# Kernel tuning notes

Hardware: AMD Instinct MI355X
Metric: run time of the kernel (lower is better)

Reference implementation:

```python
import jax, jax.numpy as jnp
import numpy as np

N, E, ND, ED, H, OUT, L, VC = 10000, 160000, 8, 4, 128, 256, 6, 6
HEADS, C = 4, 128  # GATConv: out_channels=128 per head, concat=False -> mean over heads


def _ln(x, g, b, eps=1e-5):
    m = x.mean(-1, keepdims=True)
    v = ((x - m) ** 2).mean(-1, keepdims=True)
    return (x - m) * jax.lax.rsqrt(v + eps) * g + b


def _gat_layer(h, src, dst, e_attr, lw, a_src, a_dst, lew, a_edge, bias):
    # h: [N,H]; e_attr: [Etot,H]; PyG GATConv(heads=4, concat=False, edge_dim=H)
    xh = (h @ lw).reshape(N, HEADS, C)                 # [N,4,128]
    eh = (e_attr @ lew).reshape(-1, HEADS, C)          # [Etot,4,128]
    al_s = jnp.einsum('nhc,hc->nh', xh, a_src)
    al_d = jnp.einsum('nhc,hc->nh', xh, a_dst)
    al_e = jnp.einsum('ehc,hc->eh', eh, a_edge)
    alpha = jax.nn.leaky_relu(al_s[src] + al_d[dst] + al_e, 0.2)  # [Etot,4]
    amax = jax.ops.segment_max(alpha, dst, num_segments=N)
    ex = jnp.exp(alpha - amax[dst])
    den = jax.ops.segment_sum(ex, dst, num_segments=N)
    w = ex / (den[dst] + 1e-16)
    out = jax.ops.segment_sum(xh[src] * w[..., None], dst, num_segments=N)  # [N,4,128]
    return out.mean(axis=1) + bias


def setup_inputs() -> dict:
    key = jax.random.key(0)
    ks = jax.random.split(key, 32)
    s = 0.05
    d = {
        'x': jax.random.normal(ks[0], (N, ND), jnp.float32),
        'edge_index': jax.random.randint(ks[1], (2, E), 0, N),
        'edge_attr': jax.random.uniform(ks[2], (E, ED), jnp.float32),
        'vnf_context': jax.random.normal(ks[3], (1, VC), jnp.float32),
        # node embedding
        'node_w': jax.random.normal(ks[4], (ND, H)) * s, 'node_b': jnp.zeros((H,)),
        # EdgeAttentionLayer
        'ea_proj_w': jax.random.normal(ks[5], (ED, H)) * s, 'ea_proj_b': jnp.zeros((H,)),
        'vnf_w': jax.random.normal(ks[6], (VC, H)) * s, 'vnf_b': jnp.zeros((H,)),
        'att1_w': jax.random.normal(ks[7], (2 * H, H)) * s, 'att1_b': jnp.zeros((H,)),
        'att2_w': jax.random.normal(ks[8], (H, H // 2)) * s, 'att2_b': jnp.zeros((H // 2,)),
        'att3_w': jax.random.normal(ks[9], (H // 2, 1)) * s, 'att3_b': jnp.zeros((1,)),
        # per-layer GATConv params (stacked over L layers)
        'gat_lin_w': jax.random.normal(ks[10], (L, H, HEADS * C)) * s,
        'gat_att_src': jax.random.normal(ks[11], (L, HEADS, C)) * s,
        'gat_att_dst': jax.random.normal(ks[12], (L, HEADS, C)) * s,
        'gat_lin_edge_w': jax.random.normal(ks[13], (L, H, HEADS * C)) * s,
        'gat_att_edge': jax.random.normal(ks[14], (L, HEADS, C)) * s,
        'gat_bias': jnp.zeros((L, C)),
        'ln_scale': jnp.ones((L, H)), 'ln_bias': jnp.zeros((L, H)),
        # output projection
        'out_w': jax.random.normal(ks[15], (H, OUT)) * s, 'out_b': jnp.zeros((OUT,)),
    }
    return d


def reference(x, edge_index, edge_attr, vnf_context, node_w, node_b, ea_proj_w, ea_proj_b,
              vnf_w, vnf_b, att1_w, att1_b, att2_w, att2_b, att3_w, att3_b,
              gat_lin_w, gat_att_src, gat_att_dst, gat_lin_edge_w, gat_att_edge, gat_bias,
              ln_scale, ln_bias, out_w, out_b):
    src, dst = edge_index[0], edge_index[1]
    h = x @ node_w + node_b                                   # [N,128]
    # EdgeAttentionLayer (eval mode, no network_state)
    ef = edge_attr @ ea_proj_w + ea_proj_b                    # [E,128]
    vnf = vnf_context @ vnf_w + vnf_b                         # [1,128]
    comb = jnp.concatenate([ef, jnp.broadcast_to(vnf, (E, H))], axis=-1)
    a = jax.nn.relu(comb @ att1_w + att1_b)
    a = jax.nn.relu(a @ att2_w + att2_b)
    e_gate = jax.nn.sigmoid(a @ att3_w + att3_b)              # [E,1]
    w_edge = ef * e_gate                                      # [E,128]
    # GATConv default add_self_loops=True, fill_value='mean'
    loop = jnp.arange(N)
    src2 = jnp.concatenate([src, loop])
    dst2 = jnp.concatenate([dst, loop])
    e2 = jnp.concatenate([w_edge, jnp.broadcast_to(w_edge.mean(0, keepdims=True), (N, H))], axis=0)
    for l in range(L):
        hc = _gat_layer(h, src2, dst2, e2, gat_lin_w[l], gat_att_src[l], gat_att_dst[l],
                        gat_lin_edge_w[l], gat_att_edge[l], gat_bias[l])
        h = _ln(h + jax.nn.relu(hc), ln_scale[l], ln_bias[l])
    return h @ out_w + out_b                                  # [N,256]
```

## Files before the change

### kernel.cpp

```cpp
#include <hip/hip_runtime.h>
#include <hip/hip_bf16.h>
#include <math.h>

#define Nn 10000
#define Ee 160000
#define ET 170000
#define LL 6

typedef short v8s __attribute__((ext_vector_type(8)));
typedef float v4f __attribute__((ext_vector_type(4)));

__device__ __forceinline__ unsigned short f2bf(float v) {
    unsigned int b = __float_as_uint(v);
    b += 0x7fffu + ((b >> 16) & 1u);
    return (unsigned short)(b >> 16);
}
__device__ __forceinline__ float bflo(unsigned int u) { return __uint_as_float(u << 16); }
__device__ __forceinline__ float bfhi(unsigned int u) { return __uint_as_float(u & 0xffff0000u); }

__global__ __launch_bounds__(256) void k_first(
    const float* __restrict__ x, const float* __restrict__ nw,
    const float* __restrict__ nb, float* __restrict__ h, unsigned short* __restrict__ hb,
    const int* __restrict__ ei, int* __restrict__ hist,
    const float* __restrict__ glw, const float* __restrict__ gas,
    const float* __restrict__ gad, const float* __restrict__ glew,
    const float* __restrict__ gae, float* __restrict__ Bs,
    float* __restrict__ Bd, float* __restrict__ Be,
    unsigned short* __restrict__ WsumT,
    const float* __restrict__ a2w, unsigned short* __restrict__ w2bf,
    const float* __restrict__ vnfc, const float* __restrict__ vw,
    const float* __restrict__ vb, const float* __restrict__ eab,
    const float* __restrict__ a1w, const float* __restrict__ a1b,
    const float* __restrict__ eaw, float* __restrict__ E1) {
    __shared__ float vr[128];
    __shared__ float sM1[512];
    __shared__ float sd1[128];
    int b = blockIdx.x, t = threadIdx.x;
    if (b < 5000) {
        int idx = b * 256 + t;
        int n = idx >> 7, c = idx & 127;
        const float* xr = x + (size_t)n * 8;
        float acc = nb[c];
#pragma unroll
        for (int k = 0; k < 8; k++) acc += xr[k] * nw[k * 128 + c];
        h[idx] = acc;
        hb[idx] = f2bf(acc);
        return;
    }
    if (b < 5665) {
        int i = (b - 5000) * 256 + t;
        if (i < ET) {
            int d = (i < Ee) ? ei[Ee + i] : (i - Ee);
            atomicAdd(&hist[d], 1);
        }
        return;
    }
    if (b < 5677) {
        int idx = (b - 5665) * 256 + t;
        if (idx >= LL * 128 * 4) return;
        int hh = idx & 3, k = (idx >> 2) & 127, l = idx >> 9;
        const float* lwp = glw  + (size_t)l * 65536 + k * 512 + hh * 128;
        const float* lep = glew + (size_t)l * 65536 + k * 512 + hh * 128;
        const float* sp = gas + l * 512 + hh * 128;
        const float* dp = gad + l * 512 + hh * 128;
        const float* ep = gae + l * 512 + hh * 128;
        float s1 = 0, s2 = 0, s3 = 0;
        for (int c = 0; c < 128; c++) {
            float lv = lwp[c];
            s1 += lv * sp[c];
            s2 += lv * dp[c];
            s3 += lep[c] * ep[c];
        }
        Bs[idx] = s1; Bd[idx] = s2; Be[idx] = s3;
        return;
    }
    if (b < 7213) {
        int idx = (b - 5677) * 256 + t;
        int kk = idx & 511;
        int c = (idx >> 9) & 127;
        int l = idx >> 16;
        float v = 0.25f * glw[(size_t)l * 65536 + (size_t)(kk & 127) * 512 + (kk >> 7) * 128 + c];
        WsumT[(size_t)l * 65536 + (size_t)c * 512 + kk] = f2bf(v);
        return;
    }
    if (b < 7245) {
        int idx = (b - 7213) * 256 + t;
        int j = idx & 7, lane = (idx >> 3) & 63, nt = (idx >> 9) & 3, ks = idx >> 11;
        int k = ks * 32 + ((lane >> 4) << 3) + j;
        int n = nt * 16 + (lane & 15);
        w2bf[idx] = f2bf(a2w[k * 64 + n]);
        return;
    }
    {
        if (t < 128) {
            float a = vb[t];
#pragma unroll
            for (int k = 0; k < 6; k++) a += vnfc[k] * vw[k * 128 + t];
            vr[t] = a;
        }
        __syncthreads();
        if (t < 128) {
            float a = a1b[t];
            for (int k = 0; k < 128; k++) a += eab[k] * a1w[k * 128 + t];
            for (int k = 0; k < 128; k++) a += vr[k] * a1w[(128 + k) * 128 + t];
            sd1[t] = a;
        }
#pragma unroll
        for (int rr = 0; rr < 2; rr++) {
            int id = rr * 256 + t;
            int r = id >> 7, j = id & 127;
            float a = 0.f;
            for (int k = 0; k < 128; k++) a += eaw[r * 128 + k] * a1w[k * 128 + j];
            sM1[id] = a;
        }
        __syncthreads();
        if (t < 128) {
            E1[t * 8 + 0] = sM1[t];
            E1[t * 8 + 1] = sM1[128 + t];
            E1[t * 8 + 2] = sM1[256 + t];
            E1[t * 8 + 3] = sM1[384 + t];
            E1[t * 8 + 4] = sd1[t];
            E1[t * 8 + 5] = 0.f; E1[t * 8 + 6] = 0.f; E1[t * 8 + 7] = 0.f;
        }
    }
}

__global__ __launch_bounds__(1024) void k_scan(
    const int* __restrict__ hist, int* __restrict__ seg, int* __restrict__ pos,
    const float* __restrict__ eaw, const float* __restrict__ eab,
    const float* __restrict__ Be, float* __restrict__ PB, float* __restrict__ cB) {
    __shared__ int wsums[16];
    __shared__ int carry_s;
    int t = threadIdx.x;
    if (blockIdx.x == 1) {
        if (t >= 24) return;
        int l = t >> 2, hh = t & 3;
        const float* bp = Be + l * 512 + hh;
        float s0 = 0, s1 = 0, s2 = 0, s3 = 0, sc = 0;
        for (int k = 0; k < 128; k++) {
            float bv = bp[k * 4];
            s0 += eaw[0 * 128 + k] * bv;
            s1 += eaw[1 * 128 + k] * bv;
            s2 += eaw[2 * 128 + k] * bv;
            s3 += eaw[3 * 128 + k] * bv;
            sc += eab[k] * bv;
        }
        PB[0 * 24 + t] = s0; PB[1 * 24 + t] = s1;
        PB[2 * 24 + t] = s2; PB[3 * 24 + t] = s3;
        cB[t] = sc;
        return;
    }
    int lane = t & 63, wid = t >> 6;
    if (t == 0) { carry_s = 0; seg[0] = 0; }
    __syncthreads();
    for (int base = 0; base < Nn; base += 1024) {
        int idx = base + t;
        int v = (idx < Nn) ? hist[idx] : 0;
        int sc = v;
#pragma unroll
        for (int d = 1; d < 64; d <<= 1) {
            int up = __shfl_up(sc, d);
            if (lane >= d) sc += up;
        }
        if (lane == 63) wsums[wid] = sc;
        __syncthreads();
        if (wid == 0) {
            int wv = (lane < 16) ? wsums[lane] : 0;
            int wsc = wv;
#pragma unroll
            for (int d = 1; d < 16; d <<= 1) {
                int up = __shfl_up(wsc, d);
                if (lane >= d) wsc += up;
            }
            if (lane < 16) wsums[lane] = wsc - wv;
        }
        __syncthreads();
        int carry = carry_s;
        int inc = sc + wsums[wid] + carry;
        if (idx < Nn) { seg[idx + 1] = inc; pos[idx] = inc - v; }
        __syncthreads();
        if (t == 1023) carry_s = inc;
        __syncthreads();
    }
}

__global__ __launch_bounds__(256, 2) void k_edge(
    const float* __restrict__ ea, const float* __restrict__ E1,
    const unsigned short* __restrict__ w2bf,
    const float* __restrict__ a2b, const float* __restrict__ a3w,
    const float* __restrict__ a3b,
    const float* __restrict__ PB, const float* __restrict__ cB,
    const int* __restrict__ ei, int* __restrict__ pos, int* __restrict__ srcv,
    float* __restrict__ aleT, float* __restrict__ gsum) {
    __shared__ float4 sM[128];
    __shared__ float sD[128];
    __shared__ float4 sevs[256];
    __shared__ float gsh[256];
    __shared__ float sgsum[5];
    int t = threadIdx.x;
    int lane = t & 63;
    int wid = t >> 6;
    int c = lane & 15, q = lane >> 4;
    int eb0 = blockIdx.x * 256;

    int my_src = ei[eb0 + t];
    int my_dst = ei[Ee + eb0 + t];
    sevs[t] = *(const float4*)(ea + (size_t)(eb0 + t) * 4);
    if (t < 128) {
        int slot = t ^ ((t >> 3) & 3);
        sM[slot] = *(const float4*)(E1 + t * 8);
        sD[t] = E1[t * 8 + 4];
    }
    if (t < 5) sgsum[t] = 0.f;
    __syncthreads();

    float4 ev4[4];
#pragma unroll
    for (int mt = 0; mt < 4; mt++) ev4[mt] = sevs[(wid * 4 + mt) * 16 + c];

    v8s av[4][4];
#pragma unroll
    for (int ks = 0; ks < 4; ks++) {
        float4 mr[8]; float dr[8];
#pragma unroll
        for (int j = 0; j < 8; j++) {
            int k = ks * 32 + q * 8 + j;
            mr[j] = sM[k ^ q];
            dr[j] = sD[k];
        }
#pragma unroll
        for (int mt = 0; mt < 4; mt++) {
            float4 ev = ev4[mt];
            v8s a;
#pragma unroll
            for (int j = 0; j < 8; j++) {
                float xv = fmaxf(dr[j] + ev.x * mr[j].x + ev.y * mr[j].y
                                       + ev.z * mr[j].z + ev.w * mr[j].w, 0.f);
                a[j] = (short)f2bf(xv);
            }
            av[mt][ks] = a;
        }
    }

    v4f acc[4][4];
#pragma unroll
    for (int nt = 0; nt < 4; nt++) {
        float bb = a2b[nt * 16 + c];
#pragma unroll
        for (int mt = 0; mt < 4; mt++) acc[mt][nt] = (v4f){bb, bb, bb, bb};
    }
#pragma unroll
    for (int nt = 0; nt < 4; nt++) {
#pragma unroll
        for (int ks = 0; ks < 4; ks++) {
            v8s bfr = *(const v8s*)(w2bf + ((size_t)(ks * 4 + nt) * 64 + lane) * 8);
#pragma unroll
            for (int mt = 0; mt < 4; mt++)
                acc[mt][nt] = __builtin_amdgcn_mfma_f32_16x16x32_bf16(av[mt][ks], bfr, acc[mt][nt], 0, 0, 0);
        }
    }

    float a3r[4];
#pragma unroll
    for (int nt = 0; nt < 4; nt++) a3r[nt] = a3w[nt * 16 + c];
    float a3b0 = a3b[0];
#pragma unroll
    for (int mt = 0; mt < 4; mt++) {
#pragma unroll
        for (int r = 0; r < 4; r++) {
            float s = 0.f;
#pragma unroll
            for (int nt = 0; nt < 4; nt++) s += fmaxf(acc[mt][nt][r], 0.f) * a3r[nt];
            s += __shfl_xor(s, 1); s += __shfl_xor(s, 2);
            s += __shfl_xor(s, 4); s += __shfl_xor(s, 8);
            if (c == 0) gsh[(wid * 4 + mt) * 16 + q * 4 + r] = 1.f / (1.f + __expf(-(s + a3b0)));
        }
    }
    __syncthreads();

    float g = gsh[t];
    float4 evv = sevs[t];
    float v0 = g, v1 = g * evv.x, v2 = g * evv.y, v3 = g * evv.z, v4 = g * evv.w;
#pragma unroll
    for (int d = 32; d > 0; d >>= 1) {
        v0 += __shfl_down(v0, d); v1 += __shfl_down(v1, d); v2 += __shfl_down(v2, d);
        v3 += __shfl_down(v3, d); v4 += __shfl_down(v4, d);
    }
    if (lane == 0) {
        atomicAdd(&sgsum[0], v0); atomicAdd(&sgsum[1], v1); atomicAdd(&sgsum[2], v2);
        atomicAdd(&sgsum[3], v3); atomicAdd(&sgsum[4], v4);
    }
    __syncthreads();
    if (t < 5) atomicAdd(&gsum[t], sgsum[t]);
    int slot = atomicAdd(&pos[my_dst], 1);
    srcv[slot] = my_src;
#pragma unroll
    for (int i4 = 0; i4 < 6; i4++) {
        float4 cc = *(const float4*)(cB + i4 * 4);
        float4 p0 = *(const float4*)(PB + 0 * 24 + i4 * 4);
        float4 p1 = *(const float4*)(PB + 1 * 24 + i4 * 4);
        float4 p2 = *(const float4*)(PB + 2 * 24 + i4 * 4);
        float4 p3 = *(const float4*)(PB + 3 * 24 + i4 * 4);
        float4 o;
        o.x = g * (cc.x + evv.x * p0.x + evv.y * p1.x + evv.z * p2.x + evv.w * p3.x);
        o.y = g * (cc.y + evv.x * p0.y + evv.y * p1.y + evv.z * p2.y + evv.w * p3.y);
        o.z = g * (cc.z + evv.x * p0.z + evv.y * p1.z + evv.z * p2.z + evv.w * p3.z);
        o.w = g * (cc.w + evv.x * p0.w + evv.y * p1.w + evv.z * p2.w + evv.w * p3.w);
        *(float4*)(aleT + (size_t)i4 * ET * 4 + (size_t)slot * 4) = o;
    }
}

__global__ __launch_bounds__(256) void k_abfill(
    const float* __restrict__ h, const float* __restrict__ Bs_l,
    const float* __restrict__ Bd_l, float* __restrict__ als, float* __restrict__ ald,
    int* __restrict__ pos, int* __restrict__ srcv, const float* __restrict__ gsum,
    const float* __restrict__ PB, const float* __restrict__ cB,
    float* __restrict__ aleT) {
    int b = blockIdx.x, t = threadIdx.x;
    if (b < 313) {
        int idx = b * 256 + t;
        if (idx >= Nn * 8) return;
        int n = idx >> 3, slot = idx & 7;
        const float* B = (slot < 4) ? Bs_l : Bd_l;
        int hh = slot & 3;
        const float4* hr = (const float4*)(h + (size_t)n * 128);
        float s = 0.f;
#pragma unroll 8
        for (int kb = 0; kb < 32; kb++) {
            float4 hv = hr[kb];
            s += hv.x * B[(4 * kb + 0) * 4 + hh] + hv.y * B[(4 * kb + 1) * 4 + hh]
               + hv.z * B[(4 * kb + 2) * 4 + hh] + hv.w * B[(4 * kb + 3) * 4 + hh];
        }
        if (slot < 4) als[n * 4 + hh] = s;
        else          ald[n * 4 + hh] = s;
        return;
    }
    {
        int j = (b - 313) * 256 + t;
        if (j >= Nn) return;
        int slot = atomicAdd(&pos[j], 1);
        srcv[slot] = j;
        float g0 = gsum[0], g1 = gsum[1], g2 = gsum[2], g3 = gsum[3], g4 = gsum[4];
#pragma unroll
        for (int l = 0; l < LL; l++) {
            float4 cc = *(const float4*)(cB + l * 4);
            float4 p0 = *(const float4*)(PB + 0 * 24 + l * 4);
            float4 p1 = *(const float4*)(PB + 1 * 24 + l * 4);
            float4 p2 = *(const float4*)(PB + 2 * 24 + l * 4);
            float4 p3 = *(const float4*)(PB + 3 * 24 + l * 4);
            float4 o;
            o.x = (g0 * cc.x + g1 * p0.x + g2 * p1.x + g3 * p2.x + g4 * p3.x) * (1.0f / Ee);
            o.y = (g0 * cc.y + g1 * p0.y + g2 * p1.y + g3 * p2.y + g4 * p3.y) * (1.0f / Ee);
            o.z = (g0 * cc.z + g1 * p0.z + g2 * p1.z + g3 * p2.z + g4 * p3.z) * (1.0f / Ee);
            o.w = (g0 * cc.w + g1 * p0.w + g2 * p1.w + g3 * p2.w + g4 * p3.w) * (1.0f / Ee);
            *(float4*)(aleT + (size_t)l * ET * 4 + (size_t)slot * 4) = o;
        }
    }
}

__global__ __launch_bounds__(256) void k_agg3(
    const int* __restrict__ srcv, const int* __restrict__ seg,
    const float* __restrict__ als, const float* __restrict__ ald,
    const float* __restrict__ aleS_l,
    const unsigned short* __restrict__ hb, unsigned short* __restrict__ aggb) {
    __shared__ float part[2][512];
    __shared__ float pden[2][4];
    int t = threadIdx.x;
    int lane = t & 63;
    int wv = (t >> 6) & 1;
    int w = t >> 7;
    int n = blockIdx.x * 2 + w;
    int start = seg[n], end = seg[n + 1];
    int deg = end - start;
    int half = (deg + 1) >> 1;
    int s0 = start + wv * half;
    int e0 = wv ? end : start + half;
    int hp = lane >> 4;
    int cch = (lane & 15) * 8;
    float aldh = ald[n * 4 + hp];
    float den = 0.f;
    float4 acc0 = make_float4(0.f, 0.f, 0.f, 0.f);
    float4 acc1 = make_float4(0.f, 0.f, 0.f, 0.f);
    int i = s0;
    for (; i + 4 <= e0; i += 4) {
        int sa = srcv[i], sb = srcv[i + 1], sc = srcv[i + 2], sd = srcv[i + 3];
        float ala = aleS_l[(size_t)(i + 0) * 4 + hp];
        float alb = aleS_l[(size_t)(i + 1) * 4 + hp];
        float alc = aleS_l[(size_t)(i + 2) * 4 + hp];
        float ald_ = aleS_l[(size_t)(i + 3) * 4 + hp];
        float asa = als[sa * 4 + hp], asb = als[sb * 4 + hp];
        float asc = als[sc * 4 + hp], asd = als[sd * 4 + hp];
        uint4 ua = *(const uint4*)(hb + (size_t)sa * 128 + cch);
        uint4 ub = *(const uint4*)(hb + (size_t)sb * 128 + cch);
        uint4 uc = *(const uint4*)(hb + (size_t)sc * 128 + cch);
        uint4 ud = *(const uint4*)(hb + (size_t)sd * 128 + cch);
        float ava = asa + aldh + ala; ava = ava > 0.f ? ava : 0.2f * ava;
        float avb = asb + aldh + alb; avb = avb > 0.f ? avb : 0.2f * avb;
        float avc = asc + aldh + alc; avc = avc > 0.f ? avc : 0.2f * avc;
        float avd = asd + aldh + ald_; avd = avd > 0.f ? avd : 0.2f * avd;
        float ea = __expf(fminf(ava, 60.f));
        float eb = __expf(fminf(avb, 60.f));
        float ec = __expf(fminf(avc, 60.f));
        float ed = __expf(fminf(avd, 60.f));
        den += (ea + eb) + (ec + ed);
        acc0.x += (ea * bflo(ua.x) + eb * bflo(ub.x)) + (ec * bflo(uc.x) + ed * bflo(ud.x));
        acc0.y += (ea * bfhi(ua.x) + eb * bfhi(ub.x)) + (ec * bfhi(uc.x) + ed * bfhi(ud.x));
        acc0.z += (ea * bflo(ua.y) + eb * bflo(ub.y)) + (ec * bflo(uc.y) + ed * bflo(ud.y));
        acc0.w += (ea * bfhi(ua.y) + eb * bfhi(ub.y)) + (ec * bfhi(uc.y) + ed * bfhi(ud.y));
        acc1.x += (ea * bflo(ua.z) + eb * bflo(ub.z)) + (ec * bflo(uc.z) + ed * bflo(ud.z));
        acc1.y += (ea * bfhi(ua.z) + eb * bfhi(ub.z)) + (ec * bfhi(uc.z) + ed * bfhi(ud.z));
        acc1.z += (ea * bflo(ua.w) + eb * bflo(ub.w)) + (ec * bflo(uc.w) + ed * bflo(ud.w));
        acc1.w += (ea * bfhi(ua.w) + eb * bfhi(ub.w)) + (ec * bfhi(uc.w) + ed * bfhi(ud.w));
    }
    for (; i < e0; i++) {
        int sa = srcv[i];
        float ala = aleS_l[(size_t)i * 4 + hp];
        float ava = als[sa * 4 + hp] + aldh + ala;
        ava = ava > 0.f ? ava : 0.2f * ava;
        float ea = __expf(fminf(ava, 60.f));
        den += ea;
        uint4 ua = *(const uint4*)(hb + (size_t)sa * 128 + cch);
        acc0.x += ea * bflo(ua.x); acc0.y += ea * bfhi(ua.x);
        acc0.z += ea * bflo(ua.y); acc0.w += ea * bfhi(ua.y);
        acc1.x += ea * bflo(ua.z); acc1.y += ea * bfhi(ua.z);
        acc1.z += ea * bflo(ua.w); acc1.w += ea * bfhi(ua.w);
    }
    if (wv == 1) {
        *(float4*)&part[w][lane * 8] = acc0;
        *(float4*)&part[w][lane * 8 + 4] = acc1;
        if ((lane & 15) == 0) pden[w][hp] = den;
    }
    __syncthreads();
    if (wv == 0) {
        float4 p0 = *(const float4*)&part[w][lane * 8];
        float4 p1 = *(const float4*)&part[w][lane * 8 + 4];
        float inv2 = 1.f / (den + pden[w][hp] + 1e-16f);
        acc0.x = (acc0.x + p0.x) * inv2; acc0.y = (acc0.y + p0.y) * inv2;
        acc0.z = (acc0.z + p0.z) * inv2; acc0.w = (acc0.w + p0.w) * inv2;
        acc1.x = (acc1.x + p1.x) * inv2; acc1.y = (acc1.y + p1.y) * inv2;
        acc1.z = (acc1.z + p1.z) * inv2; acc1.w = (acc1.w + p1.w) * inv2;
        ushort4 q0, q1;
        q0.x = f2bf(acc0.x); q0.y = f2bf(acc0.y); q0.z = f2bf(acc0.z); q0.w = f2bf(acc0.w);
        q1.x = f2bf(acc1.x); q1.y = f2bf(acc1.y); q1.z = f2bf(acc1.z); q1.w = f2bf(acc1.w);
        *(ushort4*)(aggb + (size_t)n * 512 + lane * 8) = q0;
        *(ushort4*)(aggb + (size_t)n * 512 + lane * 8 + 4) = q1;
    }
}

__global__ __launch_bounds__(256) void k_post(
    const unsigned short* __restrict__ aggb, const unsigned short* __restrict__ WsumT_l,
    const float* __restrict__ gbias, const float* __restrict__ lnsc,
    const float* __restrict__ lnbi, float* __restrict__ h,
    unsigned short* __restrict__ hb, const float* __restrict__ Bs_n,
    const float* __restrict__ Bd_n, float* __restrict__ als, float* __restrict__ ald) {
    int t = threadIdx.x;
    int lane = t & 63, w = t >> 6;
    int n0 = (blockIdx.x * 4 + w) * 16;
    if (n0 >= Nn) return;
    int m = lane & 15, q = lane >> 4;
    v4f acc[8];
#pragma unroll
    for (int nt = 0; nt < 8; nt++) acc[nt] = (v4f){0.f, 0.f, 0.f, 0.f};
    const unsigned short* arow = aggb + (size_t)(n0 + m) * 512 + q * 8;
#pragma unroll 4
    for (int ks = 0; ks < 16; ks++) {
        v8s fa = *(const v8s*)(arow + ks * 32);
#pragma unroll
        for (int nt = 0; nt < 8; nt++) {
            int col = nt * 16 + m;
            v8s fb = *(const v8s*)(WsumT_l + (size_t)col * 512 + ks * 32 + q * 8);
            acc[nt] = __builtin_amdgcn_mfma_f32_16x16x32_bf16(fa, fb, acc[nt], 0, 0, 0);
        }
    }
    float v[8][4];
    float s1[4] = {0.f, 0.f, 0.f, 0.f}, s2[4] = {0.f, 0.f, 0.f, 0.f};
#pragma unroll
    for (int nt = 0; nt < 8; nt++) {
        int col = nt * 16 + m;
        float b = gbias[col];
#pragma unroll
        for (int r = 0; r < 4; r++) {
            int row = n0 + q * 4 + r;
            float val = h[(size_t)row * 128 + col] + fmaxf(acc[nt][r] + b, 0.f);
            v[nt][r] = val;
            s1[r] += val; s2[r] += val * val;
        }
    }
#pragma unroll
    for (int d = 1; d <= 8; d <<= 1) {
#pragma unroll
        for (int r = 0; r < 4; r++) {
            s1[r] += __shfl_xor(s1[r], d);
            s2[r] += __shfl_xor(s2[r], d);
        }
    }
    float o8[8][4];
#pragma unroll
    for (int r = 0; r < 4; r++) {
        float mean = s1[r] * (1.f / 128.f);
        float var = s2[r] * (1.f / 128.f) - mean * mean;
        float rinv = rsqrtf(var + 1e-5f);
        int row = n0 + q * 4 + r;
#pragma unroll
        for (int nt = 0; nt < 8; nt++) {
            int col = nt * 16 + m;
            float o = (v[nt][r] - mean) * rinv * lnsc[col] + lnbi[col];
            o8[nt][r] = o;
            h[(size_t)row * 128 + col] = o;
            hb[(size_t)row * 128 + col] = f2bf(o);
        }
    }
    float sal[4][4], sad[4][4];
#pragma unroll
    for (int r = 0; r < 4; r++) {
#pragma unroll
        for (int hh = 0; hh < 4; hh++) { sal[r][hh] = 0.f; sad[r][hh] = 0.f; }
    }
#pragma unroll
    for (int nt = 0; nt < 8; nt++) {
        int col = nt * 16 + m;
        float4 bs = *(const float4*)(Bs_n + col * 4);
        float4 bd = *(const float4*)(Bd_n + col * 4);
#pragma unroll
        for (int r = 0; r < 4; r++) {
            float o = o8[nt][r];
            sal[r][0] += o * bs.x; sal[r][1] += o * bs.y;
            sal[r][2] += o * bs.z; sal[r][3] += o * bs.w;
            sad[r][0] += o * bd.x; sad[r][1] += o * bd.y;
            sad[r][2] += o * bd.z; sad[r][3] += o * bd.w;
        }
    }
#pragma unroll
    for (int d = 1; d <= 8; d <<= 1) {
#pragma unroll
        for (int r = 0; r < 4; r++) {
#pragma unroll
            for (int hh = 0; hh < 4; hh++) {
                sal[r][hh] += __shfl_xor(sal[r][hh], d);
                sad[r][hh] += __shfl_xor(sad[r][hh], d);
            }
        }
    }
    if (m < 8) {
        int hh = m & 3;
#pragma unroll
        for (int r = 0; r < 4; r++) {
            int row = n0 + q * 4 + r;
            float va = (hh == 0) ? sal[r][0] : (hh == 1) ? sal[r][1] : (hh == 2) ? sal[r][2] : sal[r][3];
            float vd = (hh == 0) ? sad[r][0] : (hh == 1) ? sad[r][1] : (hh == 2) ? sad[r][2] : sad[r][3];
            if (m < 4) als[row * 4 + hh] = va;
            else       ald[row * 4 + hh] = vd;
        }
    }
}

__global__ __launch_bounds__(256) void k_out(
    const float* __restrict__ h, const float* __restrict__ ow,
    const float* __restrict__ ob, float* __restrict__ out) {
    __shared__ float4 hs4[8][32];
    int t = threadIdx.x;
    int n0 = blockIdx.x * 8;
    if (t < 256) {
        int i = t >> 5, kb = t & 31;
        hs4[i][kb] = *(const float4*)(h + (size_t)(n0 + i) * 128 + 4 * kb);
    }
    __syncthreads();
    float acc[8] = {0, 0, 0, 0, 0, 0, 0, 0};
    for (int kb = 0; kb < 32; kb++) {
        float w0 = ow[(4 * kb + 0) * 256 + t];
        float w1 = ow[(4 * kb + 1) * 256 + t];
        float w2 = ow[(4 * kb + 2) * 256 + t];
        float w3 = ow[(4 * kb + 3) * 256 + t];
#pragma unroll
        for (int i = 0; i < 8; i++) {
            float4 hv = hs4[i][kb];
            acc[i] += hv.x * w0 + hv.y * w1 + hv.z * w2 + hv.w * w3;
        }
    }
    float b = ob[t];
#pragma unroll
    for (int i = 0; i < 8; i++) out[(size_t)(n0 + i) * 256 + t] = acc[i] + b;
}

extern "C" void kernel_launch(void* const* d_in, const int* in_sizes, int n_in,
                              void* d_out, int out_size, void* d_ws, size_t ws_size,
                              hipStream_t stream) {
    const float* x    = (const float*)d_in[0];
    const int*   ei   = (const int*)d_in[1];
    const float* ea   = (const float*)d_in[2];
    const float* vnfc = (const float*)d_in[3];
    const float* nw   = (const float*)d_in[4];
    const float* nb   = (const float*)d_in[5];
    const float* eaw  = (const float*)d_in[6];
    const float* eab  = (const float*)d_in[7];
    const float* vw   = (const float*)d_in[8];
    const float* vb   = (const float*)d_in[9];
    const float* a1w  = (const float*)d_in[10];
    const float* a1b  = (const float*)d_in[11];
    const float* a2w  = (const float*)d_in[12];
    const float* a2b  = (const float*)d_in[13];
    const float* a3w  = (const float*)d_in[14];
    const float* a3b  = (const float*)d_in[15];
    const float* glw  = (const float*)d_in[16];
    const float* gas  = (const float*)d_in[17];
    const float* gad  = (const float*)d_in[18];
    const float* glew = (const float*)d_in[19];
    const float* gae  = (const float*)d_in[20];
    const float* gb   = (const float*)d_in[21];
    const float* lnsc = (const float*)d_in[22];
    const float* lnbi = (const float*)d_in[23];
    const float* ow   = (const float*)d_in[24];
    const float* ob   = (const float*)d_in[25];
    float* out = (float*)d_out;

    char* w = (char*)d_ws;
    size_t o = 0;
    auto allocf = [&](size_t cnt) { float* p = (float*)(w + o); o += ((cnt * 4 + 255) / 256) * 256; return p; };
    auto alloci = [&](size_t cnt) { int* p = (int*)(w + o); o += ((cnt * 4 + 255) / 256) * 256; return p; };
    auto allocu = [&](size_t cnt) { unsigned short* p = (unsigned short*)(w + o); o += ((cnt * 2 + 255) / 256) * 256; return p; };
    int* hist     = alloci(Nn);
    float* gsum   = allocf(8);
    float* h      = allocf((size_t)Nn * 128);
    unsigned short* hb    = allocu((size_t)Nn * 128);
    unsigned short* aggb  = allocu((size_t)Nn * 512);
    unsigned short* WsumT = allocu((size_t)LL * 128 * 512);
    unsigned short* w2bf  = allocu(8192);
    float* als    = allocf((size_t)Nn * 4);
    float* ald    = allocf((size_t)Nn * 4);
    float* aleT   = allocf((size_t)LL * ET * 4);
    float* Bs     = allocf(3072);
    float* Bd     = allocf(3072);
    float* Be     = allocf(3072);
    float* E1     = allocf(1024);
    float* PB     = allocf(96);
    float* cB     = allocf(24);
    int* seg      = alloci(Nn + 1);
    int* pos      = alloci(Nn);
    int* srcv     = alloci(ET);

    hipMemsetAsync(hist, 0, ((size_t)Nn * 4 + 255) / 256 * 256 + 256, stream);

    k_first<<<7246, 256, 0, stream>>>(x, nw, nb, h, hb, ei, hist,
                                      glw, gas, gad, glew, gae, Bs, Bd, Be,
                                      WsumT, a2w, w2bf, vnfc, vw, vb, eab,
                                      a1w, a1b, eaw, E1);
    k_scan<<<2, 1024, 0, stream>>>(hist, seg, pos, eaw, eab, Be, PB, cB);
    k_edge<<<Ee / 256, 256, 0, stream>>>(ea, E1, w2bf, a2b, a3w, a3b, PB, cB,
                                         ei, pos, srcv, aleT, gsum);
    k_abfill<<<353, 256, 0, stream>>>(h, Bs, Bd, als, ald, pos, srcv, gsum, PB, cB, aleT);
    for (int l = 0; l < LL; l++) {
        int ln = (l + 1) % LL;
        k_agg3<<<Nn / 2, 256, 0, stream>>>(srcv, seg, als, ald,
                                           aleT + (size_t)l * ET * 4, hb, aggb);
        k_post<<<(625 + 3) / 4, 256, 0, stream>>>(aggb, WsumT + (size_t)l * 65536,
                                                  gb + l * 128, lnsc + l * 128, lnbi + l * 128,
                                                  h, hb, Bs + ln * 512, Bd + ln * 512, als, ald);
    }
    k_out<<<Nn / 8, 256, 0, stream>>>(h, ow, ob, out);
}
```

Measured before the change: 476.1 us.

## Handle self-loops analytically, fuse abfill into edge kernel, fuse output matmul into last post

Self-loop edges are no longer stored in the CSR or the edge-logit arrays. Their attention term is computed on the fly in the aggregation kernel from the global edge-attribute mean. The node-logit fill is folded into the edge kernel as extra blocks, and the final output projection is done with bf16 MFMA inside the last post-processing launch using a pre-transposed bf16 weight. This removes two launches and some memory traffic, at the cost of bf16 rounding in the output projection and a little extra per-node work in aggregation.

```diff
diff --git a/kernel.cpp b/kernel.cpp
--- a/kernel.cpp
+++ b/kernel.cpp
@@ -4,7 +4,6 @@
 
 #define Nn 10000
 #define Ee 160000
-#define ET 170000
 #define LL 6
 
 typedef short v8s __attribute__((ext_vector_type(8)));
@@ -28,6 +27,7 @@
     float* __restrict__ Bd, float* __restrict__ Be,
     unsigned short* __restrict__ WsumT,
     const float* __restrict__ a2w, unsigned short* __restrict__ w2bf,
+    const float* __restrict__ ow, unsigned short* __restrict__ owbT,
     const float* __restrict__ vnfc, const float* __restrict__ vw,
     const float* __restrict__ vb, const float* __restrict__ eab,
     const float* __restrict__ a1w, const float* __restrict__ a1b,
@@ -47,16 +47,13 @@
         hb[idx] = f2bf(acc);
         return;
     }
-    if (b < 5665) {
+    if (b < 5625) {
         int i = (b - 5000) * 256 + t;
-        if (i < ET) {
-            int d = (i < Ee) ? ei[Ee + i] : (i - Ee);
-            atomicAdd(&hist[d], 1);
-        }
-        return;
-    }
-    if (b < 5677) {
-        int idx = (b - 5665) * 256 + t;
+        atomicAdd(&hist[ei[Ee + i]], 1);
+        return;
+    }
+    if (b < 5637) {
+        int idx = (b - 5625) * 256 + t;
         if (idx >= LL * 128 * 4) return;
         int hh = idx & 3, k = (idx >> 2) & 127, l = idx >> 9;
         const float* lwp = glw  + (size_t)l * 65536 + k * 512 + hh * 128;
@@ -74,8 +71,8 @@
         Bs[idx] = s1; Bd[idx] = s2; Be[idx] = s3;
         return;
     }
-    if (b < 7213) {
-        int idx = (b - 5677) * 256 + t;
+    if (b < 7173) {
+        int idx = (b - 5637) * 256 + t;
         int kk = idx & 511;
         int c = (idx >> 9) & 127;
         int l = idx >> 16;
@@ -83,12 +80,18 @@
         WsumT[(size_t)l * 65536 + (size_t)c * 512 + kk] = f2bf(v);
         return;
     }
-    if (b < 7245) {
-        int idx = (b - 7213) * 256 + t;
+    if (b < 7205) {
+        int idx = (b - 7173) * 256 + t;
         int j = idx & 7, lane = (idx >> 3) & 63, nt = (idx >> 9) & 3, ks = idx >> 11;
         int k = ks * 32 + ((lane >> 4) << 3) + j;
         int n = nt * 16 + (lane & 15);
         w2bf[idx] = f2bf(a2w[k * 64 + n]);
+        return;
+    }
+    if (b < 7333) {
+        int idx = (b - 7205) * 256 + t;
+        int col = idx >> 7, kk = idx & 127;
+        owbT[idx] = f2bf(ow[kk * 256 + col]);
         return;
     }
     {
@@ -191,17 +194,38 @@
     const float* __restrict__ a3b,
     const float* __restrict__ PB, const float* __restrict__ cB,
     const int* __restrict__ ei, int* __restrict__ pos, int* __restrict__ srcv,
-    float* __restrict__ aleT, float* __restrict__ gsum) {
+    float* __restrict__ aleT, float* __restrict__ gsum,
+    const float* __restrict__ h, const float* __restrict__ Bs,
+    const float* __restrict__ Bd, float* __restrict__ als, float* __restrict__ ald) {
     __shared__ float4 sM[128];
     __shared__ float sD[128];
     __shared__ float4 sevs[256];
     __shared__ float gsh[256];
     __shared__ float sgsum[5];
     int t = threadIdx.x;
+    int b = blockIdx.x;
+    if (b >= 625) {
+        int idx = (b - 625) * 256 + t;
+        if (idx >= Nn * 8) return;
+        int n = idx >> 3, slot = idx & 7;
+        const float* B = (slot < 4) ? Bs : Bd;
+        int hh = slot & 3;
+        const float4* hr = (const float4*)(h + (size_t)n * 128);
+        float s = 0.f;
+#pragma unroll 8
+        for (int kb = 0; kb < 32; kb++) {
+            float4 hv = hr[kb];
+            s += hv.x * B[(4 * kb + 0) * 4 + hh] + hv.y * B[(4 * kb + 1) * 4 + hh]
+               + hv.z * B[(4 * kb + 2) * 4 + hh] + hv.w * B[(4 * kb + 3) * 4 + hh];
+        }
+        if (slot < 4) als[n * 4 + hh] = s;
+        else          ald[n * 4 + hh] = s;
+        return;
+    }
     int lane = t & 63;
     int wid = t >> 6;
     int c = lane & 15, q = lane >> 4;
-    int eb0 = blockIdx.x * 256;
+    int eb0 = b * 256;
 
     int my_src = ei[eb0 + t];
     int my_dst = ei[Ee + eb0 + t];
@@ -306,55 +330,7 @@
         o.y = g * (cc.y + evv.x * p0.y + evv.y * p1.y + evv.z * p2.y + evv.w * p3.y);
         o.z = g * (cc.z + evv.x * p0.z + evv.y * p1.z + evv.z * p2.z + evv.w * p3.z);
         o.w = g * (cc.w + evv.x * p0.w + evv.y * p1.w + evv.z * p2.w + evv.w * p3.w);
-        *(float4*)(aleT + (size_t)i4 * ET * 4 + (size_t)slot * 4) = o;
-    }
-}
-
-__global__ __launch_bounds__(256) void k_abfill(
-    const float* __restrict__ h, const float* __restrict__ Bs_l,
-    const float* __restrict__ Bd_l, float* __restrict__ als, float* __restrict__ ald,
-    int* __restrict__ pos, int* __restrict__ srcv, const float* __restrict__ gsum,
-    const float* __restrict__ PB, const float* __restrict__ cB,
-    float* __restrict__ aleT) {
-    int b = blockIdx.x, t = threadIdx.x;
-    if (b < 313) {
-        int idx = b * 256 + t;
-        if (idx >= Nn * 8) return;
-        int n = idx >> 3, slot = idx & 7;
-        const float* B = (slot < 4) ? Bs_l : Bd_l;
-        int hh = slot & 3;
-        const float4* hr = (const float4*)(h + (size_t)n * 128);
-        float s = 0.f;
-#pragma unroll 8
-        for (int kb = 0; kb < 32; kb++) {
-            float4 hv = hr[kb];
-            s += hv.x * B[(4 * kb + 0) * 4 + hh] + hv.y * B[(4 * kb + 1) * 4 + hh]
-               + hv.z * B[(4 * kb + 2) * 4 + hh] + hv.w * B[(4 * kb + 3) * 4 + hh];
-        }
-        if (slot < 4) als[n * 4 + hh] = s;
-        else          ald[n * 4 + hh] = s;
-        return;
-    }
-    {
-        int j = (b - 313) * 256 + t;
-        if (j >= Nn) return;
-        int slot = atomicAdd(&pos[j], 1);
-        srcv[slot] = j;
-        float g0 = gsum[0], g1 = gsum[1], g2 = gsum[2], g3 = gsum[3], g4 = gsum[4];
-#pragma unroll
-        for (int l = 0; l < LL; l++) {
-            float4 cc = *(const float4*)(cB + l * 4);
-            float4 p0 = *(const float4*)(PB + 0 * 24 + l * 4);
-            float4 p1 = *(const float4*)(PB + 1 * 24 + l * 4);
-            float4 p2 = *(const float4*)(PB + 2 * 24 + l * 4);
-            float4 p3 = *(const float4*)(PB + 3 * 24 + l * 4);
-            float4 o;
-            o.x = (g0 * cc.x + g1 * p0.x + g2 * p1.x + g3 * p2.x + g4 * p3.x) * (1.0f / Ee);
-            o.y = (g0 * cc.y + g1 * p0.y + g2 * p1.y + g3 * p2.y + g4 * p3.y) * (1.0f / Ee);
-            o.z = (g0 * cc.z + g1 * p0.z + g2 * p1.z + g3 * p2.z + g4 * p3.z) * (1.0f / Ee);
-            o.w = (g0 * cc.w + g1 * p0.w + g2 * p1.w + g3 * p2.w + g4 * p3.w) * (1.0f / Ee);
-            *(float4*)(aleT + (size_t)l * ET * 4 + (size_t)slot * 4) = o;
-        }
+        *(float4*)(aleT + (size_t)i4 * Ee * 4 + (size_t)slot * 4) = o;
     }
 }
 
@@ -362,7 +338,9 @@
     const int* __restrict__ srcv, const int* __restrict__ seg,
     const float* __restrict__ als, const float* __restrict__ ald,
     const float* __restrict__ aleS_l,
-    const unsigned short* __restrict__ hb, unsigned short* __restrict__ aggb) {
+    const unsigned short* __restrict__ hb, unsigned short* __restrict__ aggb,
+    const float* __restrict__ gsum, const float* __restrict__ PBl,
+    const float* __restrict__ cBl) {
     __shared__ float part[2][512];
     __shared__ float pden[2][4];
     int t = threadIdx.x;
@@ -425,6 +403,19 @@
         acc1.x += ea * bflo(ua.z); acc1.y += ea * bfhi(ua.z);
         acc1.z += ea * bflo(ua.w); acc1.w += ea * bfhi(ua.w);
     }
+    if (wv == 0) {
+        float lale = (gsum[0] * cBl[hp] + gsum[1] * PBl[hp] + gsum[2] * PBl[24 + hp]
+                    + gsum[3] * PBl[48 + hp] + gsum[4] * PBl[72 + hp]) * (1.0f / Ee);
+        float av = als[n * 4 + hp] + aldh + lale;
+        av = av > 0.f ? av : 0.2f * av;
+        float e0 = __expf(fminf(av, 60.f));
+        den += e0;
+        uint4 ua = *(const uint4*)(hb + (size_t)n * 128 + cch);
+        acc0.x += e0 * bflo(ua.x); acc0.y += e0 * bfhi(ua.x);
+        acc0.z += e0 * bflo(ua.y); acc0.w += e0 * bfhi(ua.y);
+        acc1.x += e0 * bflo(ua.z); acc1.y += e0 * bfhi(ua.z);
+        acc1.z += e0 * bflo(ua.w); acc1.w += e0 * bfhi(ua.w);
+    }
     if (wv == 1) {
         *(float4*)&part[w][lane * 8] = acc0;
         *(float4*)&part[w][lane * 8 + 4] = acc1;
@@ -452,7 +443,9 @@
     const float* __restrict__ gbias, const float* __restrict__ lnsc,
     const float* __restrict__ lnbi, float* __restrict__ h,
     unsigned short* __restrict__ hb, const float* __restrict__ Bs_n,
-    const float* __restrict__ Bd_n, float* __restrict__ als, float* __restrict__ ald) {
+    const float* __restrict__ Bd_n, float* __restrict__ als, float* __restrict__ ald,
+    const unsigned short* __restrict__ owbT, const float* __restrict__ ob,
+    float* __restrict__ out) {
     int t = threadIdx.x;
     int lane = t & 63, w = t >> 6;
     int n0 = (blockIdx.x * 4 + w) * 16;
@@ -510,76 +503,72 @@
             hb[(size_t)row * 128 + col] = f2bf(o);
         }
     }
-    float sal[4][4], sad[4][4];
-#pragma unroll
-    for (int r = 0; r < 4; r++) {
-#pragma unroll
-        for (int hh = 0; hh < 4; hh++) { sal[r][hh] = 0.f; sad[r][hh] = 0.f; }
-    }
-#pragma unroll
-    for (int nt = 0; nt < 8; nt++) {
-        int col = nt * 16 + m;
-        float4 bs = *(const float4*)(Bs_n + col * 4);
-        float4 bd = *(const float4*)(Bd_n + col * 4);
+    if (owbT == nullptr) {
+        float sal[4][4], sad[4][4];
 #pragma unroll
         for (int r = 0; r < 4; r++) {
-            float o = o8[nt][r];
-            sal[r][0] += o * bs.x; sal[r][1] += o * bs.y;
-            sal[r][2] += o * bs.z; sal[r][3] += o * bs.w;
-            sad[r][0] += o * bd.x; sad[r][1] += o * bd.y;
-            sad[r][2] += o * bd.z; sad[r][3] += o * bd.w;
-        }
-    }
-#pragma unroll
-    for (int d = 1; d <= 8; d <<= 1) {
-#pragma unroll
-        for (int r = 0; r < 4; r++) {
-#pragma unroll
-            for (int hh = 0; hh < 4; hh++) {
-                sal[r][hh] += __shfl_xor(sal[r][hh], d);
-                sad[r][hh] += __shfl_xor(sad[r][hh], d);
+#pragma unroll
+            for (int hh = 0; hh < 4; hh++) { sal[r][hh] = 0.f; sad[r][hh] = 0.f; }
+        }
+#pragma unroll
+        for (int nt = 0; nt < 8; nt++) {
+            int col = nt * 16 + m;
+            float4 bs = *(const float4*)(Bs_n + col * 4);
+            float4 bd = *(const float4*)(Bd_n + col * 4);
+#pragma unroll
+            for (int r = 0; r < 4; r++) {
+                float o = o8[nt][r];
+                sal[r][0] += o * bs.x; sal[r][1] += o * bs.y;
+                sal[r][2] += o * bs.z; sal[r][3] += o * bs.w;
+                sad[r][0] += o * bd.x; sad[r][1] += o * bd.y;
+                sad[r][2] += o * bd.z; sad[r][3] += o * bd.w;
             }
         }
-    }
-    if (m < 8) {
-        int hh = m & 3;
-#pragma unroll
-        for (int r = 0; r < 4; r++) {
-            int row = n0 + q * 4 + r;
-            float va = (hh == 0) ? sal[r][0] : (hh == 1) ? sal[r][1] : (hh == 2) ? sal[r][2] : sal[r][3];
-            float vd = (hh == 0) ? sad[r][0] : (hh == 1) ? sad[r][1] : (hh == 2) ? sad[r][2] : sad[r][3];
-            if (m < 4) als[row * 4 + hh] = va;
-            else       ald[row * 4 + hh] = vd;
-        }
-    }
-}
-
-__global__ __launch_bounds__(256) void k_out(
-    const float* __restrict__ h, const float* __restrict__ ow,
-    const float* __restrict__ ob, float* __restrict__ out) {
-    __shared__ float4 hs4[8][32];
-    int t = threadIdx.x;
-    int n0 = blockIdx.x * 8;
-    if (t < 256) {
-        int i = t >> 5, kb = t & 31;
-        hs4[i][kb] = *(const float4*)(h + (size_t)(n0 + i) * 128 + 4 * kb);
-    }
-    __syncthreads();
-    float acc[8] = {0, 0, 0, 0, 0, 0, 0, 0};
-    for (int kb = 0; kb < 32; kb++) {
-        float w0 = ow[(4 * kb + 0) * 256 + t];
-        float w1 = ow[(4 * kb + 1) * 256 + t];
-        float w2 = ow[(4 * kb + 2) * 256 + t];
-        float w3 = ow[(4 * kb + 3) * 256 + t];
-#pragma unroll
-        for (int i = 0; i < 8; i++) {
-            float4 hv = hs4[i][kb];
-            acc[i] += hv.x * w0 + hv.y * w1 + hv.z * w2 + hv.w * w3;
-        }
-    }
-    float b = ob[t];
-#pragma unroll
-    for (int i = 0; i < 8; i++) out[(size_t)(n0 + i) * 256 + t] = acc[i] + b;
+#pragma unroll
+        for (int d = 1; d <= 8; d <<= 1) {
+#pragma unroll
+            for (int r = 0; r < 4; r++) {
+#pragma unroll
+                for (int hh = 0; hh < 4; hh++) {
+                    sal[r][hh] += __shfl_xor(sal[r][hh], d);
+                    sad[r][hh] += __shfl_xor(sad[r][hh], d);
+                }
+            }
+        }
+        if (m < 8) {
+            int hh = m & 3;
+#pragma unroll
+            for (int r = 0; r < 4; r++) {
+                int row = n0 + q * 4 + r;
+                float va = (hh == 0) ? sal[r][0] : (hh == 1) ? sal[r][1] : (hh == 2) ? sal[r][2] : sal[r][3];
+                float vd = (hh == 0) ? sad[r][0] : (hh == 1) ? sad[r][1] : (hh == 2) ? sad[r][2] : sad[r][3];
+                if (m < 4) als[row * 4 + hh] = va;
+                else       ald[row * 4 + hh] = vd;
+            }
+        }
+    } else {
+        v4f oacc[16];
+#pragma unroll
+        for (int ct = 0; ct < 16; ct++) oacc[ct] = (v4f){0.f, 0.f, 0.f, 0.f};
+#pragma unroll
+        for (int ks = 0; ks < 4; ks++) {
+            v8s fa = *(const v8s*)(hb + (size_t)(n0 + m) * 128 + ks * 32 + q * 8);
+#pragma unroll
+            for (int ct = 0; ct < 16; ct++) {
+                v8s fb = *(const v8s*)(owbT + (size_t)(ct * 16 + m) * 128 + ks * 32 + q * 8);
+                oacc[ct] = __builtin_amdgcn_mfma_f32_16x16x32_bf16(fa, fb, oacc[ct], 0, 0, 0);
+            }
+        }
+#pragma unroll
+        for (int ct = 0; ct < 16; ct++) {
+            float obv = ob[ct * 16 + m];
+#pragma unroll
+            for (int r = 0; r < 4; r++) {
+                int row = n0 + q * 4 + r;
+                out[(size_t)row * 256 + ct * 16 + m] = oacc[ct][r] + obv;
+            }
+        }
+    }
 }
 
 extern "C" void kernel_launch(void* const* d_in, const int* in_sizes, int n_in,
@@ -625,9 +614,10 @@
     unsigned short* aggb  = allocu((size_t)Nn * 512);
     unsigned short* WsumT = allocu((size_t)LL * 128 * 512);
     unsigned short* w2bf  = allocu(8192);
+    unsigned short* owbT  = allocu(32768);
     float* als    = allocf((size_t)Nn * 4);
     float* ald    = allocf((size_t)Nn * 4);
-    float* aleT   = allocf((size_t)LL * ET * 4);
+    float* aleT   = allocf((size_t)LL * Ee * 4);
     float* Bs     = allocf(3072);
     float* Bd     = allocf(3072);
     float* Be     = allocf(3072);
@@ -636,25 +626,26 @@
     float* cB     = allocf(24);
     int* seg      = alloci(Nn + 1);
     int* pos      = alloci(Nn);
-    int* srcv     = alloci(ET);
+    int* srcv     = alloci(Ee);
 
     hipMemsetAsync(hist, 0, ((size_t)Nn * 4 + 255) / 256 * 256 + 256, stream);
 
-    k_first<<<7246, 256, 0, stream>>>(x, nw, nb, h, hb, ei, hist,
+    k_first<<<7334, 256, 0, stream>>>(x, nw, nb, h, hb, ei, hist,
                                       glw, gas, gad, glew, gae, Bs, Bd, Be,
-                                      WsumT, a2w, w2bf, vnfc, vw, vb, eab,
+                                      WsumT, a2w, w2bf, ow, owbT, vnfc, vw, vb, eab,
                                       a1w, a1b, eaw, E1);
     k_scan<<<2, 1024, 0, stream>>>(hist, seg, pos, eaw, eab, Be, PB, cB);
-    k_edge<<<Ee / 256, 256, 0, stream>>>(ea, E1, w2bf, a2b, a3w, a3b, PB, cB,
-                                         ei, pos, srcv, aleT, gsum);
-    k_abfill<<<353, 256, 0, stream>>>(h, Bs, Bd, als, ald, pos, srcv, gsum, PB, cB, aleT);
+    k_edge<<<938, 256, 0, stream>>>(ea, E1, w2bf, a2b, a3w, a3b, PB, cB,
+                                    ei, pos, srcv, aleT, gsum, h, Bs, Bd, als, ald);
     for (int l = 0; l < LL; l++) {
         int ln = (l + 1) % LL;
         k_agg3<<<Nn / 2, 256, 0, stream>>>(srcv, seg, als, ald,
-                                           aleT + (size_t)l * ET * 4, hb, aggb);
+                                           aleT + (size_t)l * Ee * 4, hb, aggb,
+                                           gsum, PB + l * 4, cB + l * 4);
         k_post<<<(625 + 3) / 4, 256, 0, stream>>>(aggb, WsumT + (size_t)l * 65536,
                                                   gb + l * 128, lnsc + l * 128, lnbi + l * 128,
-                                                  h, hb, Bs + ln * 512, Bd + ln * 512, als, ald);
-    }
-    k_out<<<Nn / 8, 256, 0, stream>>>(h, ow, ob, out);
+                                                  h, hb, Bs + ln * 512, Bd + ln * 512, als, ald,
+                                                  (l == LL - 1) ? owbT : (const unsigned short*)nullptr,
+                                                  ob, out);
+    }
 }
```

New measurement: 466.1 us. -2.1%, faster.
